# Performance work log

Hardware: AMD Instinct MI355X
Metric: run time of the kernel (lower is better)

## Reference

```python
import jax, jax.numpy as jnp
import numpy as np

D_MODEL = 256
N_HEADS = 8
N_LEVELS = 4
N_POINTS = 4
D_FFN = 1024
HW = 128
LQ = HW * HW
LIN = N_LEVELS * LQ
BATCH = 2
HEAD_DIM = D_MODEL // N_HEADS
SPATIAL = [(HW, HW)] * N_LEVELS  # static (H, W) per level
EPS = 1e-5


def _layer_norm(x, g, b):
    m = jnp.mean(x, axis=-1, keepdims=True)
    v = jnp.mean(jnp.square(x - m), axis=-1, keepdims=True)
    return (x - m) * jax.lax.rsqrt(v + EPS) * g + b


def _gather(v, idx):
    # v: (N, heads, HW, hd); idx: (N, heads, Lq, P) -> (N, heads, Lq, P, hd)
    N, Hh, Lq, P = idx.shape
    out = jnp.take_along_axis(v, idx.reshape(N, Hh, Lq * P)[..., None], axis=2)
    return out.reshape(N, Hh, Lq, P, -1)


def _ms_deform_attn_core(value, loc, attn):
    # value: (N, Lin, heads, hd); loc: (N, Lq, heads, L, P, 2) in [0,1]; attn: (N, Lq, heads, L, P)
    N, _, Hh, hd = value.shape
    Lq = loc.shape[1]
    out = jnp.zeros((N, Hh, Lq, hd), value.dtype)
    start = 0
    for l, (H, W) in enumerate(SPATIAL):
        v = value[:, start:start + H * W].transpose(0, 2, 1, 3)  # (N, heads, H*W, hd)
        start += H * W
        ll = loc[:, :, :, l].transpose(0, 2, 1, 3, 4)  # (N, heads, Lq, P, 2)
        # F.grid_sample(align_corners=False, padding_mode='zeros') on grid 2*loc-1:
        # pixel coord = loc * size - 0.5
        x = ll[..., 0] * W - 0.5
        y = ll[..., 1] * H - 0.5
        x0 = jnp.floor(x)
        y0 = jnp.floor(y)
        wx = x - x0
        wy = y - y0
        x0i = x0.astype(jnp.int32)
        y0i = y0.astype(jnp.int32)
        acc = jnp.zeros((N, Hh, Lq, N_POINTS, hd), value.dtype)
        for dy, wyc in ((0, 1.0 - wy), (1, wy)):
            for dx, wxc in ((0, 1.0 - wx), (1, wx)):
                xi = x0i + dx
                yi = y0i + dy
                valid = (xi >= 0) & (xi < W) & (yi >= 0) & (yi < H)
                idx = jnp.clip(yi, 0, H - 1) * W + jnp.clip(xi, 0, W - 1)
                g = _gather(v, idx)
                w = (wxc * wyc * valid).astype(value.dtype)
                acc = acc + g * w[..., None]
        aw = attn[:, :, :, l].transpose(0, 2, 1, 3)  # (N, heads, Lq, P)
        out = out + jnp.sum(acc * aw[..., None], axis=3)
    return out.transpose(0, 2, 1, 3).reshape(N, Lq, Hh * hd)


def _forward(cur_src, src_all, pos, reference_points, spatial_shape,
             W_off, b_off, W_attn, b_attn, W_val, b_val, W_out, b_out,
             gamma1, beta1, W1, b1, W2, b2, gamma2, beta2):
    N, Lq, d = cur_src.shape
    q = cur_src + pos[:, -1]                      # with_pos_embed(cur_src, pos[-1])
    inp = src_all + pos.reshape(N, -1, d)         # with_pos_embed(src_all, cat(pos, 1))
    value = (inp @ W_val + b_val).reshape(N, -1, N_HEADS, HEAD_DIM)
    off = (q @ W_off + b_off).reshape(N, Lq, N_HEADS, N_LEVELS, N_POINTS, 2)
    attn = (q @ W_attn + b_attn).reshape(N, Lq, N_HEADS, N_LEVELS * N_POINTS)
    attn = jax.nn.softmax(attn, axis=-1).reshape(N, Lq, N_HEADS, N_LEVELS, N_POINTS)
    # offset_normalizer = stack([W, H], -1)
    normalizer = jnp.stack([spatial_shape[..., 1], spatial_shape[..., 0]], -1).astype(cur_src.dtype)
    loc = reference_points[:, :, None, :, None, :] + off / normalizer[None, None, None, :, None, :]
    src2 = _ms_deform_attn_core(value, loc, attn) @ W_out + b_out
    src = _layer_norm(cur_src + src2, gamma1, beta1)   # dropout is identity in eval
    ffn = jax.nn.relu(src @ W1 + b1) @ W2 + b2
    return _layer_norm(src + ffn, gamma2, beta2)


def setup_inputs():
    key = jax.random.key(0)
    ks = jax.random.split(key, 16)
    s = 0.02
    f32 = jnp.float32
    return {
        "cur_src": jax.random.normal(ks[0], (BATCH, LQ, D_MODEL), f32),
        "src_all": jax.random.normal(ks[1], (BATCH, LIN, D_MODEL), f32),
        "pos": jax.random.normal(ks[2], (BATCH, N_LEVELS, LQ, D_MODEL), f32),
        "reference_points": jax.random.uniform(ks[3], (BATCH, LQ, N_LEVELS, 2), f32),
        "spatial_shape": jnp.array(SPATIAL, dtype=jnp.int32),
        "level_start_index": (jnp.arange(N_LEVELS) * LQ).astype(jnp.int32),
        "W_off": jax.random.normal(ks[4], (D_MODEL, N_HEADS * N_LEVELS * N_POINTS * 2), f32) * s,
        "b_off": jax.random.normal(ks[5], (N_HEADS * N_LEVELS * N_POINTS * 2,), f32) * 0.5,
        "W_attn": jax.random.normal(ks[6], (D_MODEL, N_HEADS * N_LEVELS * N_POINTS), f32) * s,
        "b_attn": jnp.zeros((N_HEADS * N_LEVELS * N_POINTS,), f32),
        "W_val": jax.random.normal(ks[7], (D_MODEL, D_MODEL), f32) * s,
        "b_val": jnp.zeros((D_MODEL,), f32),
        "W_out": jax.random.normal(ks[8], (D_MODEL, D_MODEL), f32) * s,
        "b_out": jnp.zeros((D_MODEL,), f32),
        "gamma1": jnp.ones((D_MODEL,), f32),
        "beta1": jnp.zeros((D_MODEL,), f32),
        "W1": jax.random.normal(ks[9], (D_MODEL, D_FFN), f32) * s,
        "b1": jnp.zeros((D_FFN,), f32),
        "W2": jax.random.normal(ks[10], (D_FFN, D_MODEL), f32) * s,
        "b2": jnp.zeros((D_MODEL,), f32),
        "gamma2": jnp.ones((D_MODEL,), f32),
        "beta2": jnp.zeros((D_MODEL,), f32),
    }


def reference(cur_src, src_all, pos, reference_points, spatial_shape, level_start_index,
              W_off, b_off, W_attn, b_attn, W_val, b_val, W_out, b_out,
              gamma1, beta1, W1, b1, W2, b2, gamma2, beta2):
    return _forward(cur_src, src_all, pos, reference_points, spatial_shape,
                    W_off, b_off, W_attn, b_attn, W_val, b_val, W_out, b_out,
                    gamma1, beta1, W1, b1, W2, b2, gamma2, beta2)
```

## Files before the change

### kernel.cpp

```cpp
#include <hip/hip_runtime.h>

#define LQN   16384
#define LINN  65536

typedef __attribute__((ext_vector_type(8))) short bf16x8;
typedef __attribute__((ext_vector_type(4))) float f32x4;
typedef __attribute__((ext_vector_type(4))) unsigned short bf16x4;

__device__ __forceinline__ unsigned short f2bf(float f) {
  unsigned u = __float_as_uint(f);
  u += 0x7FFFu + ((u >> 16) & 1u);
  return (unsigned short)(u >> 16);
}

__global__ __launch_bounds__(256) void wtrans6_kernel(
    const float* __restrict__ Wv, const float* __restrict__ Wo,
    const float* __restrict__ Wa, const float* __restrict__ Wu,
    const float* __restrict__ W1, const float* __restrict__ W2,
    unsigned short* __restrict__ wt) {
  int idx = blockIdx.x * 256 + threadIdx.x;
  const float* W; int K, N, base;
  if (idx < 131072) {
    if (idx < 65536) { W = Wv; K = 256; N = 256; base = 0; }
    else             { W = Wo; K = 256; N = 256; base = 65536; }
  } else if (idx < 229376) {
    if (idx < 163840) { W = Wa; K = 256; N = 128; base = 131072; }
    else              { W = Wu; K = 256; N = 256; base = 163840; }
  } else if (idx < 491520) { W = W1; K = 256; N = 1024; base = 229376; }
  else                     { W = W2; K = 1024; N = 256; base = 491520; }
  int local = idx - base;
  int n = local / K, k = local - n * K;
  wt[idx] = f2bf(W[(size_t)k * N + n]);
}

__global__ __launch_bounds__(256) void addcvt_kernel(
    const float* __restrict__ src_all, const float* __restrict__ pos,
    const float* __restrict__ cur, unsigned short* __restrict__ inp_bf,
    unsigned short* __restrict__ qb) {
  size_t i = (size_t)blockIdx.x * 256 + threadIdx.x;
  float4 a = ((const float4*)src_all)[i];
  float4 b = ((const float4*)pos)[i];
  bf16x4 o;
  o.x = f2bf(a.x + b.x); o.y = f2bf(a.y + b.y);
  o.z = f2bf(a.z + b.z); o.w = f2bf(a.w + b.w);
  ((bf16x4*)inp_bf)[i] = o;
  size_t m = i & 4194303;
  if (m >= 3145728) {
    size_t jq = (i >> 22) * 1048576 + (m - 3145728);
    float4 cc = ((const float4*)cur)[jq];
    bf16x4 o2;
    o2.x = f2bf(cc.x + b.x); o2.y = f2bf(cc.y + b.y);
    o2.z = f2bf(cc.z + b.z); o2.w = f2bf(cc.w + b.w);
    ((bf16x4*)qb)[jq] = o2;
  }
}

template <int DO_RELU, int OUT_BF16, int SPLIT, int OUT_VAL>
__global__ __launch_bounds__(256) void gemm_lds_kernel(
    const unsigned short* __restrict__ A, const unsigned short* __restrict__ Bt,
    const float* __restrict__ bias, const float* __restrict__ bias2,
    void* __restrict__ Cp, float* __restrict__ Cp2,
    int M, int N, int K, int ny) {
  __shared__ unsigned short As[128 * 64];
  __shared__ unsigned short Bs[128 * 64];
  const int bid = blockIdx.x;
  const int by = bid % ny, bx = bid / ny;
  const int m0 = bx * 128, n0 = by * 128;
  const int tid = threadIdx.x;
  const int wave = tid >> 6, lane = tid & 63;
  const int wm = (wave >> 1) * 64, wn = (wave & 1) * 64;
  const int l15 = lane & 15, quad = lane >> 4;
  const int rl = lane >> 3;
  const int cl = (lane & 7) ^ rl;

  f32x4 acc[4][4];
#pragma unroll
  for (int i = 0; i < 4; i++)
#pragma unroll
    for (int j = 0; j < 4; j++)
#pragma unroll
      for (int r = 0; r < 4; r++) acc[i][j][r] = 0.f;

  const unsigned short* Abase = A + (size_t)m0 * K + cl * 8;
  const unsigned short* Bbase = Bt + (size_t)n0 * K + cl * 8;

  for (int k0 = 0; k0 < K; k0 += 64) {
#pragma unroll
    for (int t = 0; t < 4; t++) {
      const int row = wave * 32 + t * 8 + rl;
      __builtin_amdgcn_global_load_lds(
          (const __attribute__((address_space(1))) void*)(Abase + (size_t)row * K + k0),
          (__attribute__((address_space(3))) void*)(As + (wave * 32 + t * 8) * 64),
          16, 0, 0);
      __builtin_amdgcn_global_load_lds(
          (const __attribute__((address_space(1))) void*)(Bbase + (size_t)row * K + k0),
          (__attribute__((address_space(3))) void*)(Bs + (wave * 32 + t * 8) * 64),
          16, 0, 0);
    }
    __syncthreads();
#pragma unroll
    for (int kk = 0; kk < 2; kk++) {
      bf16x8 af[4], bfr[4];
#pragma unroll
      for (int i = 0; i < 4; i++) {
        const int row = wm + i * 16 + l15;
        af[i] = *(const bf16x8*)&As[row * 64 + (((quad + 4 * kk) ^ (row & 7)) * 8)];
      }
#pragma unroll
      for (int j = 0; j < 4; j++) {
        const int row = wn + j * 16 + l15;
        bfr[j] = *(const bf16x8*)&Bs[row * 64 + (((quad + 4 * kk) ^ (row & 7)) * 8)];
      }
#pragma unroll
      for (int i = 0; i < 4; i++)
#pragma unroll
        for (int j = 0; j < 4; j++)
          acc[i][j] = __builtin_amdgcn_mfma_f32_16x16x32_bf16(af[i], bfr[j], acc[i][j], 0, 0, 0);
    }
    __syncthreads();
  }
#pragma unroll
  for (int i = 0; i < 4; i++) {
#pragma unroll
    for (int j = 0; j < 4; j++) {
      const int col = n0 + wn + j * 16 + l15;
      float bv;
      if (SPLIT) bv = (col < 256) ? bias[col] : bias2[col - 256];
      else       bv = bias[col];
#pragma unroll
      for (int r = 0; r < 4; r++) {
        const int row = m0 + wm + i * 16 + quad * 4 + r;
        float v = acc[i][j][r] + bv;
        if (DO_RELU) v = fmaxf(v, 0.f);
        if (SPLIT) {
          if (col < 256) ((float*)Cp)[(size_t)row * 256 + col] = v;
          else           Cp2[(size_t)row * 128 + (col - 256)] = v;
        } else if (OUT_BF16) {
          size_t addr;
          if (OUT_VAL)
            addr = (((size_t)(row >> 16) * 8 + (col >> 5)) * 65536 +
                    (size_t)(row & 65535)) * 32 + (col & 31);
          else
            addr = (size_t)row * N + col;
          ((unsigned short*)Cp)[addr] = f2bf(v);
        } else {
          ((float*)Cp)[(size_t)row * N + col] = v;
        }
      }
    }
  }
}

__global__ __launch_bounds__(256) void sample_kernel(
    const unsigned short* __restrict__ value, const float* __restrict__ offs,
    const float* __restrict__ attnl, const float* __restrict__ refp,
    unsigned int* __restrict__ attn_out) {
  __shared__ float wlds[32][132];
  const int tid = threadIdx.x;
  const int sub = tid >> 3;
  const int cl  = tid & 7;
  const int gb = blockIdx.x * 32 + sub;
  const int h  = gb >> 15;
  const int nl = gb & 32767;
  const int n  = nl >> 14;
  const int g  = nl * 8 + h;

  const float* lg = attnl + (size_t)nl * 128 + h * 16;
  const float2 l2 = *(const float2*)(lg + 2 * cl);
  float mx = fmaxf(l2.x, l2.y);
#pragma unroll
  for (int o = 1; o < 8; o <<= 1) mx = fmaxf(mx, __shfl_xor(mx, o, 8));
  const float e0 = __expf(l2.x - mx), e1 = __expf(l2.y - mx);
  float s = e0 + e1;
#pragma unroll
  for (int o = 1; o < 8; o <<= 1) s += __shfl_xor(s, o, 8);
  const float inv = 1.f / s;

  const float4 o4 = *(const float4*)(offs + (size_t)g * 32 + 4 * cl);
  const float2 r2 = *(const float2*)(refp + ((size_t)nl * 4 + (cl >> 1)) * 2);
#pragma unroll
  for (int q = 0; q < 2; q++) {
    const float ox = (q == 0) ? o4.x : o4.z;
    const float oy = (q == 0) ? o4.y : o4.w;
    const float aw = ((q == 0) ? e0 : e1) * inv;
    const float x = fmaf(r2.x, 128.f, ox - 0.5f);
    const float y = fmaf(r2.y, 128.f, oy - 0.5f);
    const float xf = floorf(x), yf = floorf(y);
    const float fx = x - xf, fy = y - yf;
    const int x0 = (int)xf, y0 = (int)yf;
    const float wx0 = (x0 >= 0 && x0 <= 127) ? (1.f - fx) : 0.f;
    const float wx1 = (x0 >= -1 && x0 <= 126) ? fx : 0.f;
    const float wy0 = ((y0 >= 0 && y0 <= 127) ? (1.f - fy) : 0.f) * aw;
    const float wy1 = ((y0 >= -1 && y0 <= 126) ? fy : 0.f) * aw;
    const int px = min(max(x0, 0), 126);
    const float wl = (px == x0) ? wx0 : ((px == x0 + 1) ? wx1 : 0.f);
    const float wr = (px + 1 == x0) ? wx0 : ((px == x0) ? wx1 : 0.f);
    const int yc0 = min(max(y0, 0), 127), yc1 = min(max(y0 + 1, 0), 127);
    const int lb = (cl >> 1) * 16384;
    const unsigned ot = (unsigned)(lb + yc0 * 128 + px) * 64u;
    const unsigned ob = (unsigned)(lb + yc1 * 128 + px) * 64u;
    float* wp = &wlds[sub][(2 * cl + q) * 8];
    wp[0] = wl * wy0; wp[1] = wr * wy0;
    wp[2] = wl * wy1; wp[3] = wr * wy1;
    wp[4] = __uint_as_float(ot); wp[5] = __uint_as_float(ob);
  }

  const char* hb = (const char*)value + (((size_t)(n * 8 + h)) << 22) + cl * 16;
  float a0 = 0.f, a1 = 0.f, a2 = 0.f, a3 = 0.f;
  float a4 = 0.f, a5 = 0.f, a6 = 0.f, a7 = 0.f;
#pragma unroll
  for (int p = 0; p < 16; p++) {
    const float4 w4 = *(const float4*)&wlds[sub][p * 8];
    const float2 of2 = *(const float2*)&wlds[sub][p * 8 + 4];
    const uint4 vt = *(const uint4*)(hb + __float_as_uint(of2.x));
    const uint4 vb = *(const uint4*)(hb + __float_as_uint(of2.y));
    const float wtop = (cl < 4) ? w4.x : w4.y;
    const float wbot = (cl < 4) ? w4.z : w4.w;
#define ACC8(vv, wgt)                                              \
    a0 = fmaf(wgt, __uint_as_float((vv).x << 16), a0);             \
    a1 = fmaf(wgt, __uint_as_float((vv).x & 0xFFFF0000u), a1);     \
    a2 = fmaf(wgt, __uint_as_float((vv).y << 16), a2);             \
    a3 = fmaf(wgt, __uint_as_float((vv).y & 0xFFFF0000u), a3);     \
    a4 = fmaf(wgt, __uint_as_float((vv).z << 16), a4);             \
    a5 = fmaf(wgt, __uint_as_float((vv).z & 0xFFFF0000u), a5);     \
    a6 = fmaf(wgt, __uint_as_float((vv).w << 16), a6);             \
    a7 = fmaf(wgt, __uint_as_float((vv).w & 0xFFFF0000u), a7);
    ACC8(vt, wtop)
    ACC8(vb, wbot)
#undef ACC8
  }
  a0 += __shfl_xor(a0, 4, 8); a1 += __shfl_xor(a1, 4, 8);
  a2 += __shfl_xor(a2, 4, 8); a3 += __shfl_xor(a3, 4, 8);
  a4 += __shfl_xor(a4, 4, 8); a5 += __shfl_xor(a5, 4, 8);
  a6 += __shfl_xor(a6, 4, 8); a7 += __shfl_xor(a7, 4, 8);
  if (cl < 4) {
    uint4 o;
    o.x = (unsigned)f2bf(a0) | ((unsigned)f2bf(a1) << 16);
    o.y = (unsigned)f2bf(a2) | ((unsigned)f2bf(a3) << 16);
    o.z = (unsigned)f2bf(a4) | ((unsigned)f2bf(a5) << 16);
    o.w = (unsigned)f2bf(a6) | ((unsigned)f2bf(a7) << 16);
    ((uint4*)attn_out)[(size_t)g * 4 + cl] = o;
  }
}

template <int EMIT_BF16>
__global__ __launch_bounds__(256) void ln_kernel(const float* __restrict__ x1,
                                                 const float* __restrict__ x2,
                                                 const float* __restrict__ gamma,
                                                 const float* __restrict__ beta,
                                                 float* __restrict__ out,
                                                 unsigned short* __restrict__ outb) {
  const int row = blockIdx.x * 4 + (threadIdx.x >> 6);
  const int lane = threadIdx.x & 63;
  float4 a = ((const float4*)(x1 + (size_t)row * 256))[lane];
  float4 b = ((const float4*)(x2 + (size_t)row * 256))[lane];
  float v0 = a.x + b.x, v1 = a.y + b.y, v2 = a.z + b.z, v3 = a.w + b.w;
  float s1 = v0 + v1 + v2 + v3;
  float s2 = v0 * v0 + v1 * v1 + v2 * v2 + v3 * v3;
#pragma unroll
  for (int o = 1; o < 64; o <<= 1) { s1 += __shfl_xor(s1, o); s2 += __shfl_xor(s2, o); }
  const float mean = s1 * (1.f / 256.f);
  const float var = s2 * (1.f / 256.f) - mean * mean;
  const float rstd = rsqrtf(var + 1e-5f);
  float4 gm = ((const float4*)gamma)[lane];
  float4 bt = ((const float4*)beta)[lane];
  float4 o4;
  o4.x = (v0 - mean) * rstd * gm.x + bt.x;
  o4.y = (v1 - mean) * rstd * gm.y + bt.y;
  o4.z = (v2 - mean) * rstd * gm.z + bt.z;
  o4.w = (v3 - mean) * rstd * gm.w + bt.w;
  ((float4*)(out + (size_t)row * 256))[lane] = o4;
  if (EMIT_BF16) {
    bf16x4 ob;
    ob.x = f2bf(o4.x); ob.y = f2bf(o4.y); ob.z = f2bf(o4.z); ob.w = f2bf(o4.w);
    ((bf16x4*)(outb + (size_t)row * 256))[lane] = ob;
  }
}

extern "C" void kernel_launch(void* const* d_in, const int* in_sizes, int n_in,
                              void* d_out, int out_size, void* d_ws, size_t ws_size,
                              hipStream_t stream) {
  (void)in_sizes; (void)n_in; (void)out_size; (void)ws_size;
  const float* cur_src = (const float*)d_in[0];
  const float* src_all = (const float*)d_in[1];
  const float* pos     = (const float*)d_in[2];
  const float* refp    = (const float*)d_in[3];
  const float* W_off   = (const float*)d_in[6];
  const float* b_off   = (const float*)d_in[7];
  const float* W_attn  = (const float*)d_in[8];
  const float* b_attn  = (const float*)d_in[9];
  const float* W_val   = (const float*)d_in[10];
  const float* b_val   = (const float*)d_in[11];
  const float* W_out   = (const float*)d_in[12];
  const float* b_out   = (const float*)d_in[13];
  const float* gamma1  = (const float*)d_in[14];
  const float* beta1   = (const float*)d_in[15];
  const float* W1      = (const float*)d_in[16];
  const float* b1      = (const float*)d_in[17];
  const float* W2      = (const float*)d_in[18];
  const float* b2      = (const float*)d_in[19];
  const float* gamma2  = (const float*)d_in[20];
  const float* beta2   = (const float*)d_in[21];
  float* out = (float*)d_out;

  char* ws = (char*)d_ws;
  unsigned short* value = (unsigned short*)(ws + 0);
  unsigned short* qbuf  = (unsigned short*)(ws + 67108864);
  float* offbuf         = (float*)(ws + 83886080);
  float* attnl          = (float*)(ws + 117440512);
  unsigned short* attno = (unsigned short*)(ws + 134217728);
  float* src2           = (float*)(ws + 150994944);
  float* srcb           = (float*)(ws + 184549376);
  unsigned short* wt    = (unsigned short*)(ws + 218103808);
  unsigned short* wt_val  = wt;
  unsigned short* wt_qa   = wt + 65536;
  unsigned short* wt_out  = wt + 163840;
  unsigned short* wt_1    = wt + 229376;
  unsigned short* wt_2    = wt + 491520;
  unsigned short* srcb_bf = (unsigned short*)attnl;
  unsigned short* inp_bf  = (unsigned short*)src2;

  wtrans6_kernel<<<2944, 256, 0, stream>>>(W_val, W_off, W_attn, W_out, W1, W2, wt);

  addcvt_kernel<<<32768, 256, 0, stream>>>(src_all, pos, cur_src, inp_bf, qbuf);

  gemm_lds_kernel<0, 1, 0, 1><<<2048, 256, 0, stream>>>(
      inp_bf, wt_val, b_val, nullptr, value, nullptr, 131072, 256, 256, 2);
  gemm_lds_kernel<0, 0, 1, 0><<<768, 256, 0, stream>>>(
      qbuf, wt_qa, b_off, b_attn, offbuf, attnl, 32768, 384, 256, 3);
  sample_kernel<<<8192, 256, 0, stream>>>(value, offbuf, attnl, refp,
                                          (unsigned int*)attno);
  gemm_lds_kernel<0, 0, 0, 0><<<512, 256, 0, stream>>>(
      attno, wt_out, b_out, nullptr, src2, nullptr, 32768, 256, 256, 2);
  ln_kernel<1><<<8192, 256, 0, stream>>>(cur_src, src2, gamma1, beta1, srcb, srcb_bf);
  gemm_lds_kernel<1, 1, 0, 0><<<2048, 256, 0, stream>>>(
      srcb_bf, wt_1, b1, nullptr, value, nullptr, 32768, 1024, 256, 8);
  gemm_lds_kernel<0, 0, 0, 0><<<512, 256, 0, stream>>>(
      value, wt_2, b2, nullptr, offbuf, nullptr, 32768, 256, 1024, 2);
  ln_kernel<0><<<8192, 256, 0, stream>>>(srcb, offbuf, gamma2, beta2, out, nullptr);
}
```

Measured before the change: 610.4 us.

## Fuse src+pos add and bf16 conversion into value projection GEMM

The value-projection GEMM now reads src_all and pos in fp32 directly, adds and converts them to bf16 while staging the A tile into LDS, and uses a full 256-column output tile per 512-thread block. This removes the separate add/convert pass that wrote and reread a 64 MB bf16 intermediate for all levels. The query add/convert becomes a small kernel that only touches the last level. The cost is that the A tile is loaded synchronously through registers rather than asynchronously, and each block uses more LDS.

New measurement: 605.9 us. No clear change (-0.8%).

```diff
diff --git a/kernel.cpp b/kernel.cpp
--- a/kernel.cpp
+++ b/kernel.cpp
@@ -11,6 +11,9 @@
   unsigned u = __float_as_uint(f);
   u += 0x7FFFu + ((u >> 16) & 1u);
   return (unsigned short)(u >> 16);
+}
+__device__ __forceinline__ unsigned pk2bf(float lo, float hi) {
+  return (unsigned)f2bf(lo) | ((unsigned)f2bf(hi) << 16);
 }
 
 __global__ __launch_bounds__(256) void wtrans6_kernel(
@@ -33,29 +36,115 @@
   wt[idx] = f2bf(W[(size_t)k * N + n]);
 }
 
-__global__ __launch_bounds__(256) void addcvt_kernel(
-    const float* __restrict__ src_all, const float* __restrict__ pos,
-    const float* __restrict__ cur, unsigned short* __restrict__ inp_bf,
+__global__ __launch_bounds__(256) void addcvt_q_kernel(
+    const float* __restrict__ cur, const float* __restrict__ pos,
     unsigned short* __restrict__ qb) {
-  size_t i = (size_t)blockIdx.x * 256 + threadIdx.x;
-  float4 a = ((const float4*)src_all)[i];
-  float4 b = ((const float4*)pos)[i];
+  size_t j = (size_t)blockIdx.x * 256 + threadIdx.x;
+  size_t row = j >> 6;
+  int n = (int)(row >> 14), lq = (int)(row & 16383);
+  float4 a = ((const float4*)cur)[j];
+  float4 b = ((const float4*)pos)[(((size_t)n * 4 + 3) * LQN + lq) * 64 + (j & 63)];
   bf16x4 o;
   o.x = f2bf(a.x + b.x); o.y = f2bf(a.y + b.y);
   o.z = f2bf(a.z + b.z); o.w = f2bf(a.w + b.w);
-  ((bf16x4*)inp_bf)[i] = o;
-  size_t m = i & 4194303;
-  if (m >= 3145728) {
-    size_t jq = (i >> 22) * 1048576 + (m - 3145728);
-    float4 cc = ((const float4*)cur)[jq];
-    bf16x4 o2;
-    o2.x = f2bf(cc.x + b.x); o2.y = f2bf(cc.y + b.y);
-    o2.z = f2bf(cc.z + b.z); o2.w = f2bf(cc.w + b.w);
-    ((bf16x4*)qb)[jq] = o2;
-  }
-}
-
-template <int DO_RELU, int OUT_BF16, int SPLIT, int OUT_VAL>
+  ((bf16x4*)qb)[j] = o;
+}
+
+__global__ __launch_bounds__(512) void gemmv_fused_kernel(
+    const float* __restrict__ SA, const float* __restrict__ PS,
+    const unsigned short* __restrict__ Bt, const float* __restrict__ bias,
+    unsigned short* __restrict__ Cp) {
+  __shared__ unsigned short As[128 * 64];
+  __shared__ unsigned short Bs[256 * 64];
+  const int m0 = blockIdx.x * 128;
+  const int tid = threadIdx.x;
+  const int wave = tid >> 6, lane = tid & 63;
+  const int wm = (wave >> 2) * 64;
+  const int wn = (wave & 3) * 64;
+  const int l15 = lane & 15, quad = lane >> 4;
+  const int rl = lane >> 3;
+  const int cl = (lane & 7) ^ rl;
+
+  const int ar = wave * 16 + (lane >> 2);
+  const int cb = (lane & 3) * 2;
+  const float* pa = SA + (size_t)(m0 + ar) * 256 + cb * 8;
+  const float* pb = PS + (size_t)(m0 + ar) * 256 + cb * 8;
+
+  const unsigned short* Bbase = Bt + cl * 8;
+
+  f32x4 acc[4][4];
+#pragma unroll
+  for (int i = 0; i < 4; i++)
+#pragma unroll
+    for (int j = 0; j < 4; j++)
+#pragma unroll
+      for (int r = 0; r < 4; r++) acc[i][j][r] = 0.f;
+
+  for (int k0 = 0; k0 < 256; k0 += 64) {
+#pragma unroll
+    for (int t = 0; t < 4; t++) {
+      const int row = wave * 32 + t * 8 + rl;
+      __builtin_amdgcn_global_load_lds(
+          (const __attribute__((address_space(1))) void*)(Bbase + (size_t)row * 256 + k0),
+          (__attribute__((address_space(3))) void*)(Bs + (wave * 32 + t * 8) * 64),
+          16, 0, 0);
+    }
+    float4 fa[4], fb[4];
+#pragma unroll
+    for (int u = 0; u < 4; u++) fa[u] = ((const float4*)(pa + k0))[u];
+#pragma unroll
+    for (int u = 0; u < 4; u++) fb[u] = ((const float4*)(pb + k0))[u];
+#pragma unroll
+    for (int c = 0; c < 2; c++) {
+      uint4 wv;
+      wv.x = pk2bf(fa[2 * c].x + fb[2 * c].x, fa[2 * c].y + fb[2 * c].y);
+      wv.y = pk2bf(fa[2 * c].z + fb[2 * c].z, fa[2 * c].w + fb[2 * c].w);
+      wv.z = pk2bf(fa[2 * c + 1].x + fb[2 * c + 1].x, fa[2 * c + 1].y + fb[2 * c + 1].y);
+      wv.w = pk2bf(fa[2 * c + 1].z + fb[2 * c + 1].z, fa[2 * c + 1].w + fb[2 * c + 1].w);
+      const int p = (cb + c) ^ (ar & 7);
+      *(uint4*)((char*)As + ar * 128 + p * 16) = wv;
+    }
+    __syncthreads();
+#pragma unroll
+    for (int kk = 0; kk < 2; kk++) {
+      bf16x8 af[4], bfr[4];
+#pragma unroll
+      for (int i = 0; i < 4; i++) {
+        const int row = wm + i * 16 + l15;
+        af[i] = *(const bf16x8*)&As[row * 64 + (((quad + 4 * kk) ^ (row & 7)) * 8)];
+      }
+#pragma unroll
+      for (int j = 0; j < 4; j++) {
+        const int row = wn + j * 16 + l15;
+        bfr[j] = *(const bf16x8*)&Bs[row * 64 + (((quad + 4 * kk) ^ (row & 7)) * 8)];
+      }
+#pragma unroll
+      for (int i = 0; i < 4; i++)
+#pragma unroll
+        for (int j = 0; j < 4; j++)
+          acc[i][j] = __builtin_amdgcn_mfma_f32_16x16x32_bf16(af[i], bfr[j], acc[i][j], 0, 0, 0);
+    }
+    __syncthreads();
+  }
+#pragma unroll
+  for (int i = 0; i < 4; i++) {
+#pragma unroll
+    for (int j = 0; j < 4; j++) {
+      const int col = wn + j * 16 + l15;
+      const float bv = bias[col];
+#pragma unroll
+      for (int r = 0; r < 4; r++) {
+        const int row = m0 + wm + i * 16 + quad * 4 + r;
+        const float v = acc[i][j][r] + bv;
+        const size_t addr = (((size_t)(row >> 16) * 8 + (col >> 5)) * 65536 +
+                             (size_t)(row & 65535)) * 32 + (col & 31);
+        Cp[addr] = f2bf(v);
+      }
+    }
+  }
+}
+
+template <int DO_RELU, int OUT_BF16, int SPLIT>
 __global__ __launch_bounds__(256) void gemm_lds_kernel(
     const unsigned short* __restrict__ A, const unsigned short* __restrict__ Bt,
     const float* __restrict__ bias, const float* __restrict__ bias2,
@@ -136,13 +225,7 @@
           if (col < 256) ((float*)Cp)[(size_t)row * 256 + col] = v;
           else           Cp2[(size_t)row * 128 + (col - 256)] = v;
         } else if (OUT_BF16) {
-          size_t addr;
-          if (OUT_VAL)
-            addr = (((size_t)(row >> 16) * 8 + (col >> 5)) * 65536 +
-                    (size_t)(row & 65535)) * 32 + (col & 31);
-          else
-            addr = (size_t)row * N + col;
-          ((unsigned short*)Cp)[addr] = f2bf(v);
+          ((unsigned short*)Cp)[(size_t)row * N + col] = f2bf(v);
         } else {
           ((float*)Cp)[(size_t)row * N + col] = v;
         }
@@ -318,24 +401,23 @@
   unsigned short* wt_1    = wt + 229376;
   unsigned short* wt_2    = wt + 491520;
   unsigned short* srcb_bf = (unsigned short*)attnl;
-  unsigned short* inp_bf  = (unsigned short*)src2;
 
   wtrans6_kernel<<<2944, 256, 0, stream>>>(W_val, W_off, W_attn, W_out, W1, W2, wt);
 
-  addcvt_kernel<<<32768, 256, 0, stream>>>(src_all, pos, cur_src, inp_bf, qbuf);
-
-  gemm_lds_kernel<0, 1, 0, 1><<<2048, 256, 0, stream>>>(
-      inp_bf, wt_val, b_val, nullptr, value, nullptr, 131072, 256, 256, 2);
-  gemm_lds_kernel<0, 0, 1, 0><<<768, 256, 0, stream>>>(
+  addcvt_q_kernel<<<8192, 256, 0, stream>>>(cur_src, pos, qbuf);
+
+  gemmv_fused_kernel<<<1024, 512, 0, stream>>>(src_all, pos, wt_val, b_val, value);
+
+  gemm_lds_kernel<0, 0, 1><<<768, 256, 0, stream>>>(
       qbuf, wt_qa, b_off, b_attn, offbuf, attnl, 32768, 384, 256, 3);
   sample_kernel<<<8192, 256, 0, stream>>>(value, offbuf, attnl, refp,
                                           (unsigned int*)attno);
-  gemm_lds_kernel<0, 0, 0, 0><<<512, 256, 0, stream>>>(
+  gemm_lds_kernel<0, 0, 0><<<512, 256, 0, stream>>>(
       attno, wt_out, b_out, nullptr, src2, nullptr, 32768, 256, 256, 2);
   ln_kernel<1><<<8192, 256, 0, stream>>>(cur_src, src2, gamma1, beta1, srcb, srcb_bf);
-  gemm_lds_kernel<1, 1, 0, 0><<<2048, 256, 0, stream>>>(
+  gemm_lds_kernel<1, 1, 0><<<2048, 256, 0, stream>>>(
       srcb_bf, wt_1, b1, nullptr, value, nullptr, 32768, 1024, 256, 8);
-  gemm_lds_kernel<0, 0, 0, 0><<<512, 256, 0, stream>>>(
+  gemm_lds_kernel<0, 0, 0><<<512, 256, 0, stream>>>(
       value, wt_2, b2, nullptr, offbuf, nullptr, 32768, 256, 1024, 2);
   ln_kernel<0><<<8192, 256, 0, stream>>>(srcb, offbuf, gamma2, beta2, out, nullptr);
 }
```
